# Kernel tuning notes

Measured on AMD Instinct MI355X. Metric: run time of the kernel, lower is better.

Reference implementation:

```python
import jax, jax.numpy as jnp
import numpy as np

WIN = 7                      # window_size[0] == window_size[1]
N_TOK = WIN * WIN            # 49 tokens per window
PRETRAIN = 12                # pretrain_window_size
LOG8 = float(np.log(8.0))


def _relative_position_index():
    # tf.meshgrid default 'xy' indexing == np.meshgrid default
    gh, gw = np.meshgrid(np.arange(WIN), np.arange(WIN))
    coords = np.stack([gh, gw], 0).reshape(2, -1)            # [2, N]
    rel = coords[:, :, None] - coords[:, None, :]            # [2, N, N]
    rel = rel.transpose(1, 2, 0)                             # [N, N, 2]
    ry = (rel[..., 0] + WIN - 1) * (2 * WIN - 1)
    rx = rel[..., 1] + WIN - 1
    return jnp.asarray((ry + rx).reshape(-1), dtype=jnp.int32)   # [N*N]


def _relative_coords_table():
    ch = np.arange(-(WIN - 1), WIN, dtype=np.float32)
    gh, gw = np.meshgrid(ch, ch)                             # 'xy' indexing
    t = np.stack([gh, gw], axis=-1)[None]                    # [1, 2W-1, 2W-1, 2]
    t = t / (PRETRAIN - 1)                                   # first divide
    t = t * (8.0 / (PRETRAIN - 1))                           # scale (as in source)
    t = np.sign(t) * np.log1p(np.abs(t)) / LOG8
    return jnp.asarray(t, dtype=jnp.float32)


REL_IDX = _relative_position_index()
COORDS_TABLE = _relative_coords_table()


def _l2_normalize(t, eps=1e-12):
    return t * jax.lax.rsqrt(jnp.maximum(jnp.sum(t * t, axis=-1, keepdims=True), eps))


def setup_inputs() -> dict:
    key = jax.random.key(0)
    ks = jax.random.split(key, 12)
    Bw, N, C, H, RPE_H = 2048, N_TOK, 512, 16, 512
    s = 0.02
    return {
        "x": jax.random.normal(ks[0], (Bw, N, C), jnp.float32),
        "mask": jax.random.normal(ks[1], (64, N, N), jnp.float32),
        "qkv_w": jax.random.normal(ks[2], (C, 3 * C), jnp.float32) * s,
        "q_bias": jnp.zeros((C,), jnp.float32),
        "v_bias": jnp.zeros((C,), jnp.float32),
        "logit_scale": jnp.full((H, 1, 1), np.log(10.0), jnp.float32),
        "rpe_w1": jax.random.normal(ks[3], (2, RPE_H), jnp.float32) * s,
        "rpe_b1": jnp.zeros((RPE_H,), jnp.float32),
        "rpe_w2": jax.random.normal(ks[4], (RPE_H, H), jnp.float32) * s,
        "proj_w": jax.random.normal(ks[5], (C, C), jnp.float32) * s,
        "proj_b": jnp.zeros((C,), jnp.float32),
    }


def reference(x, mask, qkv_w, q_bias, v_bias, logit_scale,
              rpe_w1, rpe_b1, rpe_w2, proj_w, proj_b):
    Bw, N, C = x.shape
    H = logit_scale.shape[0]
    hd = C // H

    qkv_bias = jnp.concatenate([q_bias, jnp.zeros_like(v_bias), v_bias])
    qkv = x @ qkv_w + qkv_bias                          # [Bw, N, 3C]
    qkv = qkv.reshape(Bw, N, 3, H, hd).transpose(2, 0, 3, 1, 4)
    q, k, v = qkv[0], qkv[1], qkv[2]                    # [Bw, H, N, hd]

    scale = jnp.exp(jnp.minimum(logit_scale, jnp.log(1.0 / 0.01)))  # [H,1,1]
    q = _l2_normalize(q)
    k = _l2_normalize(k)
    attn = jnp.einsum('bhnd,bhmd->bhnm', q, k) * scale  # [Bw, H, N, N]

    # RPE MLP on the (2W-1)^2 coords table, then gather per token pair
    h1 = jax.nn.relu(COORDS_TABLE @ rpe_w1 + rpe_b1)
    bias_table = (h1 @ rpe_w2).reshape(-1, H)           # [(2W-1)^2, H]
    pb = bias_table[REL_IDX].reshape(N, N, H).transpose(2, 0, 1)  # [H, N, N]
    attn = attn + 16.0 * jax.nn.sigmoid(pb)[None]

    nW = mask.shape[0]
    attn = attn.reshape(Bw // nW, nW, H, N, N) + mask[None, :, None]
    attn = attn.reshape(Bw, H, N, N)

    attn = jax.nn.softmax(attn, axis=-1)
    out = jnp.einsum('bhnm,bhmd->bnhd', attn, v).reshape(Bw, N, C)
    return out @ proj_w + proj_b
```

## Files before the change

kernel.cpp:

```cpp
#include <hip/hip_runtime.h>
#include <cstdint>

#define NTOK 49
#define CDIM 512
#define BW 2048
#define MROWS (BW * NTOK)
#define QKVN 1536

typedef __attribute__((ext_vector_type(4))) float f32x4;
typedef __attribute__((ext_vector_type(8))) short s16x8;
typedef __attribute__((ext_vector_type(4))) unsigned int u32x4;
typedef __attribute__((ext_vector_type(2))) unsigned int u32x2;

__device__ __forceinline__ uint16_t f2b(float f) {
  uint32_t u = __float_as_uint(f);
  u += 0x7fffu + ((u >> 16) & 1u);
  return (uint16_t)(u >> 16);
}
__device__ __forceinline__ float b2f(uint16_t h) {
  return __uint_as_float(((uint32_t)h) << 16);
}

#define GLOAD_LDS16(gp, lp)                                                    \
  __builtin_amdgcn_global_load_lds(                                            \
      (__attribute__((address_space(1))) void*)(gp),                           \
      (__attribute__((address_space(3))) void*)(lp), 16, 0, 0)

__global__ __launch_bounds__(256) void prep_all(
    const float* __restrict__ x, uint16_t* __restrict__ xb,
    const float* __restrict__ qkv_w, const float* __restrict__ proj_w,
    const float* __restrict__ q_bias, const float* __restrict__ v_bias,
    uint16_t* __restrict__ qkv_wT, uint16_t* __restrict__ proj_wT,
    float* __restrict__ qkv_bias, const float* __restrict__ w1,
    const float* __restrict__ b1, const float* __restrict__ w2,
    float* __restrict__ bias16) {
  const int bid = blockIdx.x;
  if (bid < 50176) {
    long i = ((long)bid * 256 + threadIdx.x) * 4;
    f32x4 v = *(const f32x4*)(x + i);
    uint64_t p = (uint64_t)f2b(v[0]) | ((uint64_t)f2b(v[1]) << 16) |
                 ((uint64_t)f2b(v[2]) << 32) | ((uint64_t)f2b(v[3]) << 48);
    *(uint64_t*)(xb + i) = p;
  } else if (bid < 50176 + 3072) {
    int i = (bid - 50176) * 256 + threadIdx.x;
    if (i < QKVN * CDIM) {
      int nn = i / CDIM, kk = i % CDIM;
      qkv_wT[i] = f2b(qkv_w[(long)kk * QKVN + nn]);
    }
    if (i < CDIM * CDIM) {
      int nn = i / CDIM, kk = i % CDIM;
      proj_wT[i] = f2b(proj_w[(long)kk * CDIM + nn]);
    }
    if (i < QKVN) {
      float bv = (i < 512) ? q_bias[i] : (i < 1024 ? 0.f : v_bias[i - 1024]);
      qkv_bias[i] = bv;
    }
  } else {
    int i = (bid - 53248) * 256 + threadIdx.x;
    if (i >= 169 * 16) return;
    int f = i >> 4, h = i & 15;
    float d0 = (float)((f % 13) - 6);
    float d1 = (float)((f / 13) - 6);
    const float inv_log8 = 0.4808983469629878f;
    float v0 = (d0 / 11.0f) * (8.0f / 11.0f);
    float v1 = (d1 / 11.0f) * (8.0f / 11.0f);
    float f0 = copysignf(log1pf(fabsf(v0)) * inv_log8, v0);
    if (v0 == 0.f) f0 = 0.f;
    float f1 = copysignf(log1pf(fabsf(v1)) * inv_log8, v1);
    if (v1 == 0.f) f1 = 0.f;
    float acc = 0.f;
    for (int k = 0; k < 512; ++k) {
      float h1 = fmaxf(f0 * w1[k] + f1 * w1[512 + k] + b1[k], 0.f);
      acc += h1 * w2[k * 16 + h];
    }
    bias16[i] = 16.f / (1.f + expf(-acc));
  }
}

__global__ __launch_bounds__(256) void build_T(const float* __restrict__ mask,
                                               const float* __restrict__ bias16,
                                               uint16_t* __restrict__ Tt) {
  const int w = blockIdx.x >> 4, h = blockIdx.x & 15;
  const int nt = threadIdx.x >> 6, lane = threadIdx.x & 63;
  const int cc = lane & 15, gg = lane >> 4;
  const int q = nt * 16 + cc;
  uint16_t out[16];
#pragma unroll
  for (int mt = 0; mt < 4; ++mt)
#pragma unroll
    for (int j = 0; j < 4; ++j) {
      int k = mt * 16 + gg * 4 + j;
      float T;
      if (k >= 49) T = 0.f;
      else if (q >= 49) T = 1.f;
      else {
        int ridx = (q % 7 - k % 7 + 6) * 13 + (q / 7 - k / 7 + 6);
        T = __expf(mask[(long)w * 2401 + q * 49 + k] + bias16[ridx * 16 + h]);
      }
      out[mt * 4 + j] = f2b(T);
    }
  uint16_t* dst = Tt + ((long)(w * 16 + h) * 4096 + nt * 1024 + lane * 16);
#pragma unroll
  for (int p = 0; p < 2; ++p)
    *(u32x4*)(dst + p * 8) = *(const u32x4*)(out + p * 8);
}


#define STAGE_A(tile, half, buf)                                               \
  {                                                                            \
    const uint16_t* s_ = srcA + (half) * (128L * 512) + (long)(tile) * 64;     \
    uint16_t* d_ = &lds[(buf) * 32768 + (half) * 8192 + tid * 8];              \
    GLOAD_LDS16(s_, d_);                                                       \
    GLOAD_LDS16(s_ + 64 * 512, d_ + 4096);                                     \
  }

#define STAGE_B(tile, half, buf)                                               \
  {                                                                            \
    const uint16_t* s_ = srcB + (half) * (128L * 512) + (long)(tile) * 64;     \
    uint16_t* d_ = &lds[(buf) * 32768 + 16384 + (half) * 8192 + tid * 8];      \
    GLOAD_LDS16(s_, d_);                                                       \
    GLOAD_LDS16(s_ + 64 * 512, d_ + 4096);                                     \
  }

#define VM4 asm volatile("s_waitcnt vmcnt(4)" ::: "memory");
#define VM0 asm volatile("s_waitcnt vmcnt(0)" ::: "memory");

#define PHASE(buf, q, STAGES, TAIL)                                            \
  {                                                                            \
    s16x8 a00 = *(const s16x8*)&lds[(buf)*32768 + arow + (2*(q))*1024 + ax0];  \
    s16x8 a01 = *(const s16x8*)&lds[(buf)*32768 + arow + (2*(q))*1024 + ax1];  \
    s16x8 a10 = *(const s16x8*)&lds[(buf)*32768 + arow + (2*(q)+1)*1024 + ax0];\
    s16x8 a11 = *(const s16x8*)&lds[(buf)*32768 + arow + (2*(q)+1)*1024 + ax1];\
    if ((q) == 0) {                                                            \
      _Pragma("unroll")                                                        \
      for (int nf = 0; nf < 4; ++nf) {                                         \
        bfr0[nf] = *(const s16x8*)&lds[(buf)*32768 + brow_ + nf*1024 + ax0];   \
        bfr1[nf] = *(const s16x8*)&lds[(buf)*32768 + brow_ + nf*1024 + ax1];   \
      }                                                                        \
    }                                                                          \
    STAGES                                                                     \
    __builtin_amdgcn_s_barrier();                                              \
    asm volatile("s_waitcnt lgkmcnt(0)" ::: "memory");                         \
    __builtin_amdgcn_sched_barrier(0);                                         \
    __builtin_amdgcn_s_setprio(1);                                             \
    _Pragma("unroll")                                                          \
    for (int nf = 0; nf < 4; ++nf) {                                           \
      acc[2*(q)][nf] = __builtin_amdgcn_mfma_f32_16x16x32_bf16(                \
          a00, bfr0[nf], acc[2*(q)][nf], 0, 0, 0);                             \
      acc[2*(q)][nf] = __builtin_amdgcn_mfma_f32_16x16x32_bf16(                \
          a01, bfr1[nf], acc[2*(q)][nf], 0, 0, 0);                             \
      acc[2*(q)+1][nf] = __builtin_amdgcn_mfma_f32_16x16x32_bf16(              \
          a10, bfr0[nf], acc[2*(q)+1][nf], 0, 0, 0);                           \
      acc[2*(q)+1][nf] = __builtin_amdgcn_mfma_f32_16x16x32_bf16(              \
          a11, bfr1[nf], acc[2*(q)+1][nf], 0, 0, 0);                           \
    }                                                                          \
    __builtin_amdgcn_s_setprio(0);                                             \
    TAIL                                                                       \
    __builtin_amdgcn_s_barrier();                                              \
  }

template <int EPI>
__global__ __launch_bounds__(512, 2) void gemm8p(const uint16_t* __restrict__ A,
                                                 const uint16_t* __restrict__ BT,
                                                 const float* __restrict__ bias,
                                                 void* __restrict__ Cout,
                                                 int N, int ntn) {
  __shared__ uint16_t lds[2 * 32768];
  const int tid = threadIdx.x;
  const int wave = tid >> 6, lane = tid & 63;
  const int wm = wave >> 2, wn = wave & 3;
  const int c = lane & 15, g = lane >> 4;

  const int bid = blockIdx.x;
  const int nwg = gridDim.x;
  const int wg = (bid & 7) * (nwg >> 3) + (bid >> 3);
  const int mt = wg / ntn, nt = wg % ntn;
  const long brow = (long)mt * 256;
  const int bcol = nt * 256;

  const int lr0 = tid >> 3;
  const int chunk = tid & 7;
  const int scol = (chunk ^ (lr0 & 7)) * 8;
  const uint16_t* srcA = A + (brow + lr0) * 512 + scol;
  const uint16_t* srcB = BT + ((long)bcol + lr0) * 512 + scol;

  const int arow = wm * 8192 + c * 64;
  const int brow_ = 16384 + (wn >> 1) * 8192 + ((wn & 1) * 64 + c) * 64;
  const int ax0 = (g * 8) ^ ((c & 7) * 8);
  const int ax1 = (32 + g * 8) ^ ((c & 7) * 8);

  f32x4 acc[8][4];
#pragma unroll
  for (int i = 0; i < 8; ++i)
#pragma unroll
    for (int j = 0; j < 4; ++j) acc[i][j] = f32x4{0.f, 0.f, 0.f, 0.f};
  s16x8 bfr0[4], bfr1[4];

  STAGE_A(0, 0, 0); STAGE_A(0, 1, 0);
  STAGE_B(0, 0, 0); STAGE_B(0, 1, 0);
  STAGE_B(1, 0, 1); STAGE_B(1, 1, 1);
  asm volatile("s_waitcnt vmcnt(4)" ::: "memory");
  __builtin_amdgcn_s_barrier();

  for (int i = 0; i < 3; ++i) {
    const int t0 = 2 * i;
    PHASE(0, 0, STAGE_A(t0 + 1, 0, 1), )
    PHASE(0, 1, STAGE_A(t0 + 1, 1, 1), )
    PHASE(0, 2, STAGE_B(t0 + 2, 0, 0), )
    PHASE(0, 3, STAGE_B(t0 + 2, 1, 0), VM4)
    PHASE(1, 0, STAGE_A(t0 + 2, 0, 0), )
    PHASE(1, 1, STAGE_A(t0 + 2, 1, 0), )
    PHASE(1, 2, STAGE_B(t0 + 3, 0, 1), )
    PHASE(1, 3, STAGE_B(t0 + 3, 1, 1), VM4)
  }
  PHASE(0, 0, STAGE_A(7, 0, 1), )
  PHASE(0, 1, STAGE_A(7, 1, 1), )
  PHASE(0, 2, , )
  PHASE(0, 3, , VM0)
  PHASE(1, 0, , )
  PHASE(1, 1, , )
  PHASE(1, 2, , )
  PHASE(1, 3, , )

#pragma unroll
  for (int mf = 0; mf < 8; ++mf) {
#pragma unroll
    for (int nf = 0; nf < 4; ++nf) {
      const int col = bcol + wn * 64 + nf * 16 + c;
      const float bv = bias[col];
#pragma unroll
      for (int r = 0; r < 4; ++r) {
        const long grow = brow + wm * 128 + mf * 16 + g * 4 + r;
        const float v = acc[mf][nf][r] + bv;
        if (EPI == 0)
          ((uint16_t*)Cout)[grow * N + col] = f2b(v);
        else
          ((float*)Cout)[grow * N + col] = v;
      }
    }
  }
}

__global__ __launch_bounds__(256, 4) void attn_mfma(
    const uint16_t* __restrict__ qkv,
    const float* __restrict__ logit_scale,
    const uint16_t* __restrict__ Tt,
    uint16_t* __restrict__ outb) {
  __shared__ uint16_t Vs[4][2048];
  const int tid = threadIdx.x;
  const int wave = tid >> 6, lane = tid & 63;
  const int g = lane >> 4, c = lane & 15;
  const int b = blockIdx.x >> 2;
  const int h = ((blockIdx.x & 3) << 2) | wave;
  const long rbase = (long)b * 49;

  uint16_t* vdst = Vs[wave];
#pragma unroll
  for (int i = 0; i < 4; ++i) {
    int chunk = i * 64 + lane;
    int row = chunk >> 2, part = chunk & 3;
    if (row > 48) { row = 0; part = 0; }
    GLOAD_LDS16(qkv + (rbase + row) * QKVN + 1024 + h * 32 + part * 8,
                vdst + i * 512 + lane * 8);
  }

  const long qoff = rbase * QKVN + h * 32;
  s16x8 kf[4], qf[4];
#pragma unroll
  for (int t = 0; t < 4; ++t) {
    int row = t * 16 + c;
    s16x8 kv = {}, qv = {};
    if (row < 49) {
      qv = *(const s16x8*)(qkv + qoff + (long)row * QKVN + g * 8);
      kv = *(const s16x8*)(qkv + qoff + (long)row * QKVN + 512 + g * 8);
    }
    float kfv[8], qfv[8];
    float kss = 0.f, qss = 0.f;
#pragma unroll
    for (int m = 0; m < 8; ++m) {
      kfv[m] = b2f((uint16_t)kv[m]); kss += kfv[m] * kfv[m];
      qfv[m] = b2f((uint16_t)qv[m]); qss += qfv[m] * qfv[m];
    }
    kss += __shfl_xor(kss, 16); kss += __shfl_xor(kss, 32);
    qss += __shfl_xor(qss, 16); qss += __shfl_xor(qss, 32);
    float kr = rsqrtf(fmaxf(kss, 1e-12f));
    float qr = rsqrtf(fmaxf(qss, 1e-12f));
#pragma unroll
    for (int m = 0; m < 8; ++m) {
      kv[m] = (short)f2b(kfv[m] * kr);
      qv[m] = (short)f2b(qfv[m] * qr);
    }
    kf[t] = kv; qf[t] = qv;
  }

  const float scale = __expf(fminf(logit_scale[h], 4.6051702f));
  const uint16_t* Tbase = Tt + (long)(((b & 63) * 16 + h)) * 4096;

  u32x4 aT[4][2];
  const int dstlo = (c + 16 * (g >> 1)) * 4;
  const int dsthi = (c + 16 * (2 + (g >> 1))) * 4;
  const bool godd = (g & 1) != 0;
  const bool low = (lane < 32);

#pragma unroll
  for (int nt = 0; nt < 4; ++nt) {
    s16x8 t01 = *(const s16x8*)(Tbase + nt * 1024 + lane * 16);
    s16x8 t23 = *(const s16x8*)(Tbase + nt * 1024 + lane * 16 + 8);

    f32x4 sv[4];
    __builtin_amdgcn_s_setprio(1);
#pragma unroll
    for (int mt = 0; mt < 4; ++mt)
      sv[mt] = __builtin_amdgcn_mfma_f32_16x16x32_bf16(
          kf[mt], qf[nt], f32x4{0.f, 0.f, 0.f, 0.f}, 0, 0, 0);
    __builtin_amdgcn_s_setprio(0);

    float mx = -3.0e38f;
#pragma unroll
    for (int mt = 0; mt < 4; ++mt)
#pragma unroll
      for (int j = 0; j < 4; ++j) {
        sv[mt][j] *= scale;
        mx = fmaxf(mx, sv[mt][j]);
      }
    mx = fmaxf(mx, __shfl_xor(mx, 16));
    mx = fmaxf(mx, __shfl_xor(mx, 32));
    float sum = 0.f;
#pragma unroll
    for (int mt = 0; mt < 4; ++mt) {
#pragma unroll
      for (int j = 0; j < 4; ++j) {
        uint16_t tb = (uint16_t)((mt < 2) ? t01[mt * 4 + j] : t23[(mt - 2) * 4 + j]);
        float e = b2f(tb) * __expf(sv[mt][j] - mx);
        sv[mt][j] = e; sum += e;
      }
    }
    sum += __shfl_xor(sum, 16);
    sum += __shfl_xor(sum, 32);
    float inv = 1.0f / sum;
#pragma unroll
    for (int mt = 0; mt < 4; ++mt)
#pragma unroll
      for (int j = 0; j < 4; ++j) sv[mt][j] *= inv;

    unsigned pk[4][2];
#pragma unroll
    for (int mt = 0; mt < 4; ++mt) {
      pk[mt][0] = (unsigned)f2b(sv[mt][0]) | ((unsigned)f2b(sv[mt][1]) << 16);
      pk[mt][1] = (unsigned)f2b(sv[mt][2]) | ((unsigned)f2b(sv[mt][3]) << 16);
    }
#pragma unroll
    for (int x = 0; x < 2; ++x)
#pragma unroll
      for (int K = 0; K < 2; ++K) {
        int vA = godd ? (int)pk[2 * K + 1][x] : (int)pk[2 * K][x];
        int dA = godd ? dsthi : dstlo;
        int rA = __builtin_amdgcn_ds_permute(dA, vA);
        int vB = godd ? (int)pk[2 * K][x] : (int)pk[2 * K + 1][x];
        int dB = godd ? dstlo : dsthi;
        int rB = __builtin_amdgcn_ds_permute(dB, vB);
        aT[nt][K][x]     = (unsigned)(low ? rA : rB);
        aT[nt][K][2 + x] = (unsigned)(low ? rB : rA);
      }
  }

  asm volatile("s_waitcnt vmcnt(0)" ::: "memory");

  f32x4 o[4][2];
#pragma unroll
  for (int qt = 0; qt < 4; ++qt)
#pragma unroll
    for (int dt = 0; dt < 2; ++dt) o[qt][dt] = f32x4{0.f, 0.f, 0.f, 0.f};

#pragma unroll
  for (int ks = 0; ks < 2; ++ks) {
    s16x8 vf[2];
#pragma unroll
    for (int dt = 0; dt < 2; ++dt) {
      int d = dt * 16 + c;
      s16x8 vv;
#pragma unroll
      for (int jj = 0; jj < 8; ++jj) {
        int k = ks * 32 + g * 8 + jj;
        vv[jj] = (short)vdst[k * 32 + d];
      }
      vf[dt] = vv;
    }
    __builtin_amdgcn_s_setprio(1);
#pragma unroll
    for (int qt = 0; qt < 4; ++qt) {
      s16x8 pf = __builtin_bit_cast(s16x8, aT[qt][ks]);
#pragma unroll
      for (int dt = 0; dt < 2; ++dt)
        o[qt][dt] = __builtin_amdgcn_mfma_f32_16x16x32_bf16(pf, vf[dt],
                                                            o[qt][dt], 0, 0, 0);
    }
    __builtin_amdgcn_s_setprio(0);
  }

#pragma unroll
  for (int qt = 0; qt < 4; ++qt) {
    int q0 = qt * 16 + g * 4;
#pragma unroll
    for (int dt = 0; dt < 2; ++dt)
#pragma unroll
      for (int j = 0; j < 4; ++j) {
        int q = q0 + j;
        if (q < 49) vdst[q * 40 + dt * 16 + c] = f2b(o[qt][dt][j]);
      }
  }
#pragma unroll
  for (int i = 0; i < 4; ++i) {
    int row = i * 16 + (lane >> 2);
    if (row < 49) {
      int chunk = lane & 3;
      s16x8 ov = *(const s16x8*)&vdst[row * 40 + chunk * 8];
      *(s16x8*)(outb + (rbase + row) * 512 + h * 32 + chunk * 8) = ov;
    }
  }
}

extern "C" void kernel_launch(void* const* d_in, const int* in_sizes, int n_in,
                              void* d_out, int out_size, void* d_ws,
                              size_t ws_size, hipStream_t stream) {
  const float* x = (const float*)d_in[0];
  const float* mask = (const float*)d_in[1];
  const float* qkv_w = (const float*)d_in[2];
  const float* q_bias = (const float*)d_in[3];
  const float* v_bias = (const float*)d_in[4];
  const float* logit_scale = (const float*)d_in[5];
  const float* rpe_w1 = (const float*)d_in[6];
  const float* rpe_b1 = (const float*)d_in[7];
  const float* rpe_w2 = (const float*)d_in[8];
  const float* proj_w = (const float*)d_in[9];
  const float* proj_b = (const float*)d_in[10];

  char* ws = (char*)d_ws;
  uint16_t* xb       = (uint16_t*)ws;
  uint16_t* qkvbuf   = (uint16_t*)(ws + 102760448L);
  uint16_t* qkv_wT   = (uint16_t*)(ws + 411041792L);
  uint16_t* proj_wT  = (uint16_t*)(ws + 412614656L);
  float*    qkv_bias = (float*)(ws + 413138944L);
  float*    bias16   = (float*)(ws + 413145088L);
  uint16_t* Tt       = (uint16_t*)(ws + 413155904L);

  prep_all<<<53259, 256, 0, stream>>>(x, xb, qkv_w, proj_w, q_bias, v_bias,
                                      qkv_wT, proj_wT, qkv_bias, rpe_w1,
                                      rpe_b1, rpe_w2, bias16);
  build_T<<<1024, 256, 0, stream>>>(mask, bias16, Tt);

  gemm8p<0><<<2352, 512, 0, stream>>>(xb, qkv_wT, qkv_bias, qkvbuf, QKVN, 6);
  attn_mfma<<<8192, 256, 0, stream>>>(qkvbuf, logit_scale, Tt, xb);
  gemm8p<1><<<784, 512, 0, stream>>>(xb, proj_wT, proj_b, d_out, CDIM, 2);
}
```

Measured before the change: 503.0 us.

## Fuse fp32-to-bf16 input conversion into QKV GEMM A-tile loading

Removes the separate pass that converted x to bf16 and instead loads fp32 x tiles into registers inside the QKV GEMM, converting them with packed bf16 conversion instructions before writing to LDS. This eliminates a full read/write pass over the large activation tensor. In exchange, the GEMM reads twice the bytes per A tile (repeated across N-tiles), uses more registers, and replaces asynchronous global-to-LDS loads for A with register-staged loads and explicit LDS writes.

```diff
diff --git a/kernel.cpp b/kernel.cpp
--- a/kernel.cpp
+++ b/kernel.cpp
@@ -20,6 +20,11 @@
 __device__ __forceinline__ float b2f(uint16_t h) {
   return __uint_as_float(((uint32_t)h) << 16);
 }
+__device__ __forceinline__ unsigned cvtpk(float lo, float hi) {
+  unsigned r;
+  asm("v_cvt_pk_bf16_f32 %0, %1, %2" : "=v"(r) : "v"(lo), "v"(hi));
+  return r;
+}
 
 #define GLOAD_LDS16(gp, lp)                                                    \
   __builtin_amdgcn_global_load_lds(                                            \
@@ -27,7 +32,6 @@
       (__attribute__((address_space(3))) void*)(lp), 16, 0, 0)
 
 __global__ __launch_bounds__(256) void prep_all(
-    const float* __restrict__ x, uint16_t* __restrict__ xb,
     const float* __restrict__ qkv_w, const float* __restrict__ proj_w,
     const float* __restrict__ q_bias, const float* __restrict__ v_bias,
     uint16_t* __restrict__ qkv_wT, uint16_t* __restrict__ proj_wT,
@@ -35,14 +39,8 @@
     const float* __restrict__ b1, const float* __restrict__ w2,
     float* __restrict__ bias16) {
   const int bid = blockIdx.x;
-  if (bid < 50176) {
-    long i = ((long)bid * 256 + threadIdx.x) * 4;
-    f32x4 v = *(const f32x4*)(x + i);
-    uint64_t p = (uint64_t)f2b(v[0]) | ((uint64_t)f2b(v[1]) << 16) |
-                 ((uint64_t)f2b(v[2]) << 32) | ((uint64_t)f2b(v[3]) << 48);
-    *(uint64_t*)(xb + i) = p;
-  } else if (bid < 50176 + 3072) {
-    int i = (bid - 50176) * 256 + threadIdx.x;
+  if (bid < 3072) {
+    int i = bid * 256 + threadIdx.x;
     if (i < QKVN * CDIM) {
       int nn = i / CDIM, kk = i % CDIM;
       qkv_wT[i] = f2b(qkv_w[(long)kk * QKVN + nn]);
@@ -56,7 +54,7 @@
       qkv_bias[i] = bv;
     }
   } else {
-    int i = (bid - 53248) * 256 + threadIdx.x;
+    int i = (bid - 3072) * 256 + threadIdx.x;
     if (i >= 169 * 16) return;
     int f = i >> 4, h = i & 15;
     float d0 = (float)((f % 13) - 6);
@@ -122,8 +120,32 @@
     GLOAD_LDS16(s_ + 64 * 512, d_ + 4096);                                     \
   }
 
+#define AL(p, tile, half)                                                      \
+  {                                                                            \
+    const float* s_ = srcAf + (half) * (128L * 512) + (long)(tile) * 64;       \
+    p##0 = *(const f32x4*)(s_);                                                \
+    p##1 = *(const f32x4*)(s_ + 4);                                            \
+    p##2 = *(const f32x4*)(s_ + 64 * 512);                                     \
+    p##3 = *(const f32x4*)(s_ + 64 * 512 + 4);                                 \
+  }
+
+#define CVT_WRITE(buf, half, p)                                                \
+  {                                                                            \
+    u32x4 w0_ = {cvtpk(p##0[0], p##0[1]), cvtpk(p##0[2], p##0[3]),             \
+                 cvtpk(p##1[0], p##1[1]), cvtpk(p##1[2], p##1[3])};            \
+    *(u32x4*)&lds[(buf) * 32768 + (half) * 8192 + tid * 8] = w0_;              \
+    u32x4 w1_ = {cvtpk(p##2[0], p##2[1]), cvtpk(p##2[2], p##2[3]),             \
+                 cvtpk(p##3[0], p##3[1]), cvtpk(p##3[2], p##3[3])};            \
+    *(u32x4*)&lds[(buf) * 32768 + (half) * 8192 + tid * 8 + 4096] = w1_;       \
+  }
+
+#define VM8 asm volatile("s_waitcnt vmcnt(8)" ::: "memory");
 #define VM4 asm volatile("s_waitcnt vmcnt(4)" ::: "memory");
 #define VM0 asm volatile("s_waitcnt vmcnt(0)" ::: "memory");
+#define LGK0 asm volatile("s_waitcnt lgkmcnt(0)" ::: "memory");
+
+#define CW(buf)                                                                \
+  CVT_WRITE(buf, 0, pa) CVT_WRITE(buf, 1, pb) LGK0
 
 #define PHASE(buf, q, STAGES, TAIL)                                            \
   {                                                                            \
@@ -159,11 +181,10 @@
     __builtin_amdgcn_s_barrier();                                              \
   }
 
-template <int EPI>
 __global__ __launch_bounds__(512, 2) void gemm8p(const uint16_t* __restrict__ A,
                                                  const uint16_t* __restrict__ BT,
                                                  const float* __restrict__ bias,
-                                                 void* __restrict__ Cout,
+                                                 float* __restrict__ Cout,
                                                  int N, int ntn) {
   __shared__ uint16_t lds[2 * 32768];
   const int tid = threadIdx.x;
@@ -199,7 +220,7 @@
   STAGE_A(0, 0, 0); STAGE_A(0, 1, 0);
   STAGE_B(0, 0, 0); STAGE_B(0, 1, 0);
   STAGE_B(1, 0, 1); STAGE_B(1, 1, 1);
-  asm volatile("s_waitcnt vmcnt(4)" ::: "memory");
+  VM4
   __builtin_amdgcn_s_barrier();
 
   for (int i = 0; i < 3; ++i) {
@@ -231,11 +252,87 @@
 #pragma unroll
       for (int r = 0; r < 4; ++r) {
         const long grow = brow + wm * 128 + mf * 16 + g * 4 + r;
-        const float v = acc[mf][nf][r] + bv;
-        if (EPI == 0)
-          ((uint16_t*)Cout)[grow * N + col] = f2b(v);
-        else
-          ((float*)Cout)[grow * N + col] = v;
+        Cout[grow * N + col] = acc[mf][nf][r] + bv;
+      }
+    }
+  }
+}
+
+__global__ __launch_bounds__(512, 2) void gemm8p_xf32(
+    const float* __restrict__ Af, const uint16_t* __restrict__ BT,
+    const float* __restrict__ bias, uint16_t* __restrict__ Cout,
+    int N, int ntn) {
+  __shared__ uint16_t lds[2 * 32768];
+  const int tid = threadIdx.x;
+  const int wave = tid >> 6, lane = tid & 63;
+  const int wm = wave >> 2, wn = wave & 3;
+  const int c = lane & 15, g = lane >> 4;
+
+  const int bid = blockIdx.x;
+  const int nwg = gridDim.x;
+  const int wg = (bid & 7) * (nwg >> 3) + (bid >> 3);
+  const int mt = wg / ntn, nt = wg % ntn;
+  const long brow = (long)mt * 256;
+  const int bcol = nt * 256;
+
+  const int lr0 = tid >> 3;
+  const int chunk = tid & 7;
+  const int scol = (chunk ^ (lr0 & 7)) * 8;
+  const float* srcAf = Af + (brow + lr0) * 512 + scol;
+  const uint16_t* srcB = BT + ((long)bcol + lr0) * 512 + scol;
+
+  const int arow = wm * 8192 + c * 64;
+  const int brow_ = 16384 + (wn >> 1) * 8192 + ((wn & 1) * 64 + c) * 64;
+  const int ax0 = (g * 8) ^ ((c & 7) * 8);
+  const int ax1 = (32 + g * 8) ^ ((c & 7) * 8);
+
+  f32x4 acc[8][4];
+#pragma unroll
+  for (int i = 0; i < 8; ++i)
+#pragma unroll
+    for (int j = 0; j < 4; ++j) acc[i][j] = f32x4{0.f, 0.f, 0.f, 0.f};
+  s16x8 bfr0[4], bfr1[4];
+  f32x4 pa0, pa1, pa2, pa3, pb0, pb1, pb2, pb3;
+
+  AL(pa, 0, 0) AL(pb, 0, 1)
+  STAGE_B(0, 0, 0); STAGE_B(0, 1, 0);
+  STAGE_B(1, 0, 1); STAGE_B(1, 1, 1);
+  VM8
+  CVT_WRITE(0, 0, pa) CVT_WRITE(0, 1, pb)
+  VM4
+  LGK0
+  __builtin_amdgcn_s_barrier();
+
+  for (int i = 0; i < 3; ++i) {
+    const int t0 = 2 * i;
+    PHASE(0, 0, AL(pa, t0 + 1, 0), )
+    PHASE(0, 1, AL(pb, t0 + 1, 1), )
+    PHASE(0, 2, STAGE_B(t0 + 2, 0, 0), )
+    PHASE(0, 3, STAGE_B(t0 + 2, 1, 0), VM4 CW(1))
+    PHASE(1, 0, AL(pa, t0 + 2, 0), )
+    PHASE(1, 1, AL(pb, t0 + 2, 1), )
+    PHASE(1, 2, STAGE_B(t0 + 3, 0, 1), )
+    PHASE(1, 3, STAGE_B(t0 + 3, 1, 1), VM4 CW(0))
+  }
+  PHASE(0, 0, AL(pa, 7, 0), )
+  PHASE(0, 1, AL(pb, 7, 1), )
+  PHASE(0, 2, , )
+  PHASE(0, 3, , VM0 CW(1))
+  PHASE(1, 0, , )
+  PHASE(1, 1, , )
+  PHASE(1, 2, , )
+  PHASE(1, 3, , )
+
+#pragma unroll
+  for (int mf = 0; mf < 8; ++mf) {
+#pragma unroll
+    for (int nf = 0; nf < 4; ++nf) {
+      const int col = bcol + wn * 64 + nf * 16 + c;
+      const float bv = bias[col];
+#pragma unroll
+      for (int r = 0; r < 4; ++r) {
+        const long grow = brow + wm * 128 + mf * 16 + g * 4 + r;
+        Cout[grow * N + col] = f2b(acc[mf][nf][r] + bv);
       }
     }
   }
@@ -444,12 +541,12 @@
   float*    bias16   = (float*)(ws + 413145088L);
   uint16_t* Tt       = (uint16_t*)(ws + 413155904L);
 
-  prep_all<<<53259, 256, 0, stream>>>(x, xb, qkv_w, proj_w, q_bias, v_bias,
-                                      qkv_wT, proj_wT, qkv_bias, rpe_w1,
-                                      rpe_b1, rpe_w2, bias16);
+  prep_all<<<3083, 256, 0, stream>>>(qkv_w, proj_w, q_bias, v_bias, qkv_wT,
+                                     proj_wT, qkv_bias, rpe_w1, rpe_b1, rpe_w2,
+                                     bias16);
   build_T<<<1024, 256, 0, stream>>>(mask, bias16, Tt);
 
-  gemm8p<0><<<2352, 512, 0, stream>>>(xb, qkv_wT, qkv_bias, qkvbuf, QKVN, 6);
+  gemm8p_xf32<<<2352, 512, 0, stream>>>(x, qkv_wT, qkv_bias, qkvbuf, QKVN, 6);
   attn_mfma<<<8192, 256, 0, stream>>>(qkvbuf, logit_scale, Tt, xb);
-  gemm8p<1><<<784, 512, 0, stream>>>(xb, proj_wT, proj_b, d_out, CDIM, 2);
-}
+  gemm8p<<<784, 512, 0, stream>>>(xb, proj_wT, proj_b, (float*)d_out, CDIM, 2);
+}
```

New measurement: 514.5 us. 1.02x slower.

## Process two windows per attention block with prefetched V and packed bf16 convert

Applied to the files above, without the earlier changes.

Each attention block now handles two windows (b1 and b1+1024, which share the same mask/bias table slice), halving the grid size. V for both windows is loaded into LDS up front so the second window's load overlaps the first window's compute, and the T-table base is reused. The manual bf16 rounding of probabilities is replaced with a packed v_cvt_pk_bf16_f32 instruction. LDS per block doubles, which may reduce occupancy, and fewer blocks may reduce latency hiding.

```diff
diff --git a/kernel.cpp b/kernel.cpp
--- a/kernel.cpp
+++ b/kernel.cpp
@@ -19,6 +19,11 @@
 }
 __device__ __forceinline__ float b2f(uint16_t h) {
   return __uint_as_float(((uint32_t)h) << 16);
+}
+__device__ __forceinline__ unsigned cvtpk(float lo, float hi) {
+  unsigned r;
+  asm("v_cvt_pk_bf16_f32 %0, %1, %2" : "=v"(r) : "v"(lo), "v"(hi));
+  return r;
 }
 
 #define GLOAD_LDS16(gp, lp)                                                    \
@@ -199,7 +204,7 @@
   STAGE_A(0, 0, 0); STAGE_A(0, 1, 0);
   STAGE_B(0, 0, 0); STAGE_B(0, 1, 0);
   STAGE_B(1, 0, 1); STAGE_B(1, 1, 1);
-  asm volatile("s_waitcnt vmcnt(4)" ::: "memory");
+  VM4
   __builtin_amdgcn_s_barrier();
 
   for (int i = 0; i < 3; ++i) {
@@ -246,176 +251,184 @@
     const float* __restrict__ logit_scale,
     const uint16_t* __restrict__ Tt,
     uint16_t* __restrict__ outb) {
-  __shared__ uint16_t Vs[4][2048];
+  __shared__ uint16_t Vs[4][2][2048];
   const int tid = threadIdx.x;
   const int wave = tid >> 6, lane = tid & 63;
   const int g = lane >> 4, c = lane & 15;
-  const int b = blockIdx.x >> 2;
+  const int b1 = blockIdx.x >> 2;
   const int h = ((blockIdx.x & 3) << 2) | wave;
-  const long rbase = (long)b * 49;
-
-  uint16_t* vdst = Vs[wave];
-#pragma unroll
-  for (int i = 0; i < 4; ++i) {
-    int chunk = i * 64 + lane;
-    int row = chunk >> 2, part = chunk & 3;
-    if (row > 48) { row = 0; part = 0; }
-    GLOAD_LDS16(qkv + (rbase + row) * QKVN + 1024 + h * 32 + part * 8,
-                vdst + i * 512 + lane * 8);
-  }
-
-  const long qoff = rbase * QKVN + h * 32;
-  s16x8 kf[4], qf[4];
-#pragma unroll
-  for (int t = 0; t < 4; ++t) {
-    int row = t * 16 + c;
-    s16x8 kv = {}, qv = {};
-    if (row < 49) {
-      qv = *(const s16x8*)(qkv + qoff + (long)row * QKVN + g * 8);
-      kv = *(const s16x8*)(qkv + qoff + (long)row * QKVN + 512 + g * 8);
-    }
-    float kfv[8], qfv[8];
-    float kss = 0.f, qss = 0.f;
-#pragma unroll
-    for (int m = 0; m < 8; ++m) {
-      kfv[m] = b2f((uint16_t)kv[m]); kss += kfv[m] * kfv[m];
-      qfv[m] = b2f((uint16_t)qv[m]); qss += qfv[m] * qfv[m];
-    }
-    kss += __shfl_xor(kss, 16); kss += __shfl_xor(kss, 32);
-    qss += __shfl_xor(qss, 16); qss += __shfl_xor(qss, 32);
-    float kr = rsqrtf(fmaxf(kss, 1e-12f));
-    float qr = rsqrtf(fmaxf(qss, 1e-12f));
-#pragma unroll
-    for (int m = 0; m < 8; ++m) {
-      kv[m] = (short)f2b(kfv[m] * kr);
-      qv[m] = (short)f2b(qfv[m] * qr);
-    }
-    kf[t] = kv; qf[t] = qv;
+
+#pragma unroll
+  for (int w2 = 0; w2 < 2; ++w2) {
+    const long rb = (long)(b1 + w2 * 1024) * 49;
+    uint16_t* vdst = Vs[wave][w2];
+#pragma unroll
+    for (int i = 0; i < 4; ++i) {
+      int chunk = i * 64 + lane;
+      int row = chunk >> 2, part = chunk & 3;
+      if (row > 48) { row = 0; part = 0; }
+      GLOAD_LDS16(qkv + (rb + row) * QKVN + 1024 + h * 32 + part * 8,
+                  vdst + i * 512 + lane * 8);
+    }
   }
 
   const float scale = __expf(fminf(logit_scale[h], 4.6051702f));
-  const uint16_t* Tbase = Tt + (long)(((b & 63) * 16 + h)) * 4096;
-
-  u32x4 aT[4][2];
+  const uint16_t* Tbase = Tt + (long)(((b1 & 63) * 16 + h)) * 4096;
   const int dstlo = (c + 16 * (g >> 1)) * 4;
   const int dsthi = (c + 16 * (2 + (g >> 1))) * 4;
   const bool godd = (g & 1) != 0;
   const bool low = (lane < 32);
 
 #pragma unroll
-  for (int nt = 0; nt < 4; ++nt) {
-    s16x8 t01 = *(const s16x8*)(Tbase + nt * 1024 + lane * 16);
-    s16x8 t23 = *(const s16x8*)(Tbase + nt * 1024 + lane * 16 + 8);
-
-    f32x4 sv[4];
-    __builtin_amdgcn_s_setprio(1);
-#pragma unroll
-    for (int mt = 0; mt < 4; ++mt)
-      sv[mt] = __builtin_amdgcn_mfma_f32_16x16x32_bf16(
-          kf[mt], qf[nt], f32x4{0.f, 0.f, 0.f, 0.f}, 0, 0, 0);
-    __builtin_amdgcn_s_setprio(0);
-
-    float mx = -3.0e38f;
-#pragma unroll
-    for (int mt = 0; mt < 4; ++mt)
-#pragma unroll
-      for (int j = 0; j < 4; ++j) {
-        sv[mt][j] *= scale;
-        mx = fmaxf(mx, sv[mt][j]);
-      }
-    mx = fmaxf(mx, __shfl_xor(mx, 16));
-    mx = fmaxf(mx, __shfl_xor(mx, 32));
-    float sum = 0.f;
-#pragma unroll
-    for (int mt = 0; mt < 4; ++mt) {
-#pragma unroll
-      for (int j = 0; j < 4; ++j) {
-        uint16_t tb = (uint16_t)((mt < 2) ? t01[mt * 4 + j] : t23[(mt - 2) * 4 + j]);
-        float e = b2f(tb) * __expf(sv[mt][j] - mx);
-        sv[mt][j] = e; sum += e;
-      }
-    }
-    sum += __shfl_xor(sum, 16);
-    sum += __shfl_xor(sum, 32);
-    float inv = 1.0f / sum;
-#pragma unroll
-    for (int mt = 0; mt < 4; ++mt)
-#pragma unroll
-      for (int j = 0; j < 4; ++j) sv[mt][j] *= inv;
-
-    unsigned pk[4][2];
-#pragma unroll
-    for (int mt = 0; mt < 4; ++mt) {
-      pk[mt][0] = (unsigned)f2b(sv[mt][0]) | ((unsigned)f2b(sv[mt][1]) << 16);
-      pk[mt][1] = (unsigned)f2b(sv[mt][2]) | ((unsigned)f2b(sv[mt][3]) << 16);
-    }
-#pragma unroll
-    for (int x = 0; x < 2; ++x)
-#pragma unroll
-      for (int K = 0; K < 2; ++K) {
-        int vA = godd ? (int)pk[2 * K + 1][x] : (int)pk[2 * K][x];
-        int dA = godd ? dsthi : dstlo;
-        int rA = __builtin_amdgcn_ds_permute(dA, vA);
-        int vB = godd ? (int)pk[2 * K][x] : (int)pk[2 * K + 1][x];
-        int dB = godd ? dstlo : dsthi;
-        int rB = __builtin_amdgcn_ds_permute(dB, vB);
-        aT[nt][K][x]     = (unsigned)(low ? rA : rB);
-        aT[nt][K][2 + x] = (unsigned)(low ? rB : rA);
-      }
-  }
-
-  asm volatile("s_waitcnt vmcnt(0)" ::: "memory");
-
-  f32x4 o[4][2];
-#pragma unroll
-  for (int qt = 0; qt < 4; ++qt)
-#pragma unroll
-    for (int dt = 0; dt < 2; ++dt) o[qt][dt] = f32x4{0.f, 0.f, 0.f, 0.f};
-
-#pragma unroll
-  for (int ks = 0; ks < 2; ++ks) {
-    s16x8 vf[2];
-#pragma unroll
-    for (int dt = 0; dt < 2; ++dt) {
-      int d = dt * 16 + c;
-      s16x8 vv;
-#pragma unroll
-      for (int jj = 0; jj < 8; ++jj) {
-        int k = ks * 32 + g * 8 + jj;
-        vv[jj] = (short)vdst[k * 32 + d];
-      }
-      vf[dt] = vv;
-    }
-    __builtin_amdgcn_s_setprio(1);
+  for (int w2 = 0; w2 < 2; ++w2) {
+    const long rbase = (long)(b1 + w2 * 1024) * 49;
+    uint16_t* vdst = Vs[wave][w2];
+
+    const long qoff = rbase * QKVN + h * 32;
+    s16x8 kf[4], qf[4];
+#pragma unroll
+    for (int t = 0; t < 4; ++t) {
+      int row = t * 16 + c;
+      s16x8 kv = {}, qv = {};
+      if (row < 49) {
+        qv = *(const s16x8*)(qkv + qoff + (long)row * QKVN + g * 8);
+        kv = *(const s16x8*)(qkv + qoff + (long)row * QKVN + 512 + g * 8);
+      }
+      float kfv[8], qfv[8];
+      float kss = 0.f, qss = 0.f;
+#pragma unroll
+      for (int m = 0; m < 8; ++m) {
+        kfv[m] = b2f((uint16_t)kv[m]); kss += kfv[m] * kfv[m];
+        qfv[m] = b2f((uint16_t)qv[m]); qss += qfv[m] * qfv[m];
+      }
+      kss += __shfl_xor(kss, 16); kss += __shfl_xor(kss, 32);
+      qss += __shfl_xor(qss, 16); qss += __shfl_xor(qss, 32);
+      float kr = rsqrtf(fmaxf(kss, 1e-12f));
+      float qr = rsqrtf(fmaxf(qss, 1e-12f));
+#pragma unroll
+      for (int m = 0; m < 8; ++m) {
+        kv[m] = (short)f2b(kfv[m] * kr);
+        qv[m] = (short)f2b(qfv[m] * qr);
+      }
+      kf[t] = kv; qf[t] = qv;
+    }
+
+    u32x4 aT[4][2];
+#pragma unroll
+    for (int nt = 0; nt < 4; ++nt) {
+      s16x8 t01 = *(const s16x8*)(Tbase + nt * 1024 + lane * 16);
+      s16x8 t23 = *(const s16x8*)(Tbase + nt * 1024 + lane * 16 + 8);
+
+      f32x4 sv[4];
+      __builtin_amdgcn_s_setprio(1);
+#pragma unroll
+      for (int mt = 0; mt < 4; ++mt)
+        sv[mt] = __builtin_amdgcn_mfma_f32_16x16x32_bf16(
+            kf[mt], qf[nt], f32x4{0.f, 0.f, 0.f, 0.f}, 0, 0, 0);
+      __builtin_amdgcn_s_setprio(0);
+
+      float mx = -3.0e38f;
+#pragma unroll
+      for (int mt = 0; mt < 4; ++mt)
+#pragma unroll
+        for (int j = 0; j < 4; ++j) {
+          sv[mt][j] *= scale;
+          mx = fmaxf(mx, sv[mt][j]);
+        }
+      mx = fmaxf(mx, __shfl_xor(mx, 16));
+      mx = fmaxf(mx, __shfl_xor(mx, 32));
+      float sum = 0.f;
+#pragma unroll
+      for (int mt = 0; mt < 4; ++mt) {
+#pragma unroll
+        for (int j = 0; j < 4; ++j) {
+          uint16_t tb = (uint16_t)((mt < 2) ? t01[mt * 4 + j] : t23[(mt - 2) * 4 + j]);
+          float e = b2f(tb) * __expf(sv[mt][j] - mx);
+          sv[mt][j] = e; sum += e;
+        }
+      }
+      sum += __shfl_xor(sum, 16);
+      sum += __shfl_xor(sum, 32);
+      float inv = 1.0f / sum;
+#pragma unroll
+      for (int mt = 0; mt < 4; ++mt)
+#pragma unroll
+        for (int j = 0; j < 4; ++j) sv[mt][j] *= inv;
+
+      unsigned pk[4][2];
+#pragma unroll
+      for (int mt = 0; mt < 4; ++mt) {
+        pk[mt][0] = cvtpk(sv[mt][0], sv[mt][1]);
+        pk[mt][1] = cvtpk(sv[mt][2], sv[mt][3]);
+      }
+#pragma unroll
+      for (int x = 0; x < 2; ++x)
+#pragma unroll
+        for (int K = 0; K < 2; ++K) {
+          int vA = godd ? (int)pk[2 * K + 1][x] : (int)pk[2 * K][x];
+          int dA = godd ? dsthi : dstlo;
+          int rA = __builtin_amdgcn_ds_permute(dA, vA);
+          int vB = godd ? (int)pk[2 * K][x] : (int)pk[2 * K + 1][x];
+          int dB = godd ? dstlo : dsthi;
+          int rB = __builtin_amdgcn_ds_permute(dB, vB);
+          aT[nt][K][x]     = (unsigned)(low ? rA : rB);
+          aT[nt][K][2 + x] = (unsigned)(low ? rB : rA);
+        }
+    }
+
+    if (w2 == 0) { asm volatile("s_waitcnt vmcnt(0)" ::: "memory"); }
+
+    f32x4 o[4][2];
+#pragma unroll
+    for (int qt = 0; qt < 4; ++qt)
+#pragma unroll
+      for (int dt = 0; dt < 2; ++dt) o[qt][dt] = f32x4{0.f, 0.f, 0.f, 0.f};
+
+#pragma unroll
+    for (int ks = 0; ks < 2; ++ks) {
+      s16x8 vf[2];
+#pragma unroll
+      for (int dt = 0; dt < 2; ++dt) {
+        int d = dt * 16 + c;
+        s16x8 vv;
+#pragma unroll
+        for (int jj = 0; jj < 8; ++jj) {
+          int k = ks * 32 + g * 8 + jj;
+          vv[jj] = (short)vdst[k * 32 + d];
+        }
+        vf[dt] = vv;
+      }
+      __builtin_amdgcn_s_setprio(1);
+#pragma unroll
+      for (int qt = 0; qt < 4; ++qt) {
+        s16x8 pf = __builtin_bit_cast(s16x8, aT[qt][ks]);
+#pragma unroll
+        for (int dt = 0; dt < 2; ++dt)
+          o[qt][dt] = __builtin_amdgcn_mfma_f32_16x16x32_bf16(pf, vf[dt],
+                                                              o[qt][dt], 0, 0, 0);
+      }
+      __builtin_amdgcn_s_setprio(0);
+    }
+
 #pragma unroll
     for (int qt = 0; qt < 4; ++qt) {
-      s16x8 pf = __builtin_bit_cast(s16x8, aT[qt][ks]);
+      int q0 = qt * 16 + g * 4;
 #pragma unroll
       for (int dt = 0; dt < 2; ++dt)
-        o[qt][dt] = __builtin_amdgcn_mfma_f32_16x16x32_bf16(pf, vf[dt],
-                                                            o[qt][dt], 0, 0, 0);
-    }
-    __builtin_amdgcn_s_setprio(0);
-  }
-
-#pragma unroll
-  for (int qt = 0; qt < 4; ++qt) {
-    int q0 = qt * 16 + g * 4;
-#pragma unroll
-    for (int dt = 0; dt < 2; ++dt)
-#pragma unroll
-      for (int j = 0; j < 4; ++j) {
-        int q = q0 + j;
-        if (q < 49) vdst[q * 40 + dt * 16 + c] = f2b(o[qt][dt][j]);
-      }
-  }
-#pragma unroll
-  for (int i = 0; i < 4; ++i) {
-    int row = i * 16 + (lane >> 2);
-    if (row < 49) {
-      int chunk = lane & 3;
-      s16x8 ov = *(const s16x8*)&vdst[row * 40 + chunk * 8];
-      *(s16x8*)(outb + (rbase + row) * 512 + h * 32 + chunk * 8) = ov;
+#pragma unroll
+        for (int j = 0; j < 4; ++j) {
+          int q = q0 + j;
+          if (q < 49) vdst[q * 40 + dt * 16 + c] = f2b(o[qt][dt][j]);
+        }
+    }
+#pragma unroll
+    for (int i = 0; i < 4; ++i) {
+      int row = i * 16 + (lane >> 2);
+      if (row < 49) {
+        int chunk = lane & 3;
+        s16x8 ov = *(const s16x8*)&vdst[row * 40 + chunk * 8];
+        *(s16x8*)(outb + (rbase + row) * 512 + h * 32 + chunk * 8) = ov;
+      }
     }
   }
 }
@@ -450,6 +463,6 @@
   build_T<<<1024, 256, 0, stream>>>(mask, bias16, Tt);
 
   gemm8p<0><<<2352, 512, 0, stream>>>(xb, qkv_wT, qkv_bias, qkvbuf, QKVN, 6);
-  attn_mfma<<<8192, 256, 0, stream>>>(qkvbuf, logit_scale, Tt, xb);
+  attn_mfma<<<4096, 256, 0, stream>>>(qkvbuf, logit_scale, Tt, xb);
   gemm8p<1><<<784, 512, 0, stream>>>(xb, proj_wT, proj_b, d_out, CDIM, 2);
 }
```

Result: no change. 508.6 us (+1.1%).
